# Kernel tuning notes

Measured on AMD Instinct MI355X. Metric: run time of the kernel, lower is better.

The kernel has to match this reference:

```python
import jax, jax.numpy as jnp
import numpy as np

L, D, H, DFF = 12, 768, 12, 3072
DH = D // H
EPS = 1e-5


def _layer_norm(x, g, b):
    # manual LN as in source: biased variance, eps inside sqrt
    mean = jnp.mean(x, axis=-1, keepdims=True)
    var = jnp.mean((x - mean) ** 2, axis=-1, keepdims=True)
    return g * (x - mean) / jnp.sqrt(var + EPS) + b


def setup_inputs() -> dict:
    key = jax.random.key(0)
    ks = jax.random.split(key, 10)
    x = jax.random.normal(ks[0], (8, 512, D), dtype=jnp.float32)
    mask = jnp.zeros((8, 1, 1, 512), dtype=jnp.float32)
    s = 0.02
    Wq = jax.random.normal(ks[1], (L, D, D), jnp.float32) * s
    Wk = jax.random.normal(ks[2], (L, D, D), jnp.float32) * s
    Wv = jax.random.normal(ks[3], (L, D, D), jnp.float32) * s
    Wo = jax.random.normal(ks[4], (L, D, D), jnp.float32) * s
    W1 = jax.random.normal(ks[5], (L, DFF, D), jnp.float32) * s
    W2 = jax.random.normal(ks[6], (L, D, DFF), jnp.float32) * s
    z = lambda *sh: jnp.zeros(sh, jnp.float32)
    o = lambda *sh: jnp.ones(sh, jnp.float32)
    return {
        'x': x, 'mask': mask,
        'Wq': Wq, 'bq': z(L, D), 'Wk': Wk, 'bk': z(L, D), 'Wv': Wv, 'bv': z(L, D),
        'Wo': Wo, 'bo': z(L, D), 'g1': o(L, D), 'b1': z(L, D),
        'W1': W1, 'bf1': z(L, DFF), 'W2': W2, 'bf2': z(L, D),
        'g2': o(L, D), 'b2': z(L, D),
    }


def reference(x, mask, Wq, bq, Wk, bk, Wv, bv, Wo, bo, g1, b1, W1, bf1, W2, bf2, g2, b2):
    B, S, _ = x.shape
    scale = 1.0 / jnp.sqrt(jnp.float32(DH))

    def layer(h, p):
        wq, pq, wk, pk, wv, pv, wo, po, gg1, bb1, w1, pf1, w2, pf2, gg2, bb2 = p
        # Dense: x @ W^T + b
        q = (h @ wq.T + pq).reshape(B, S, H, DH).transpose(0, 2, 1, 3)  # [B,H,S,dh]
        k = (h @ wk.T + pk).reshape(B, S, H, DH).transpose(0, 2, 1, 3)
        v = (h @ wv.T + pv).reshape(B, S, H, DH).transpose(0, 2, 1, 3)
        scores = jnp.einsum('bhqd,bhkd->bhqk', q, k) * scale
        scores = scores + mask * -1e9
        attn = jax.nn.softmax(scores, axis=-1)
        ctx = jnp.einsum('bhqk,bhkd->bhqd', attn, v)
        ctx = ctx.transpose(0, 2, 1, 3).reshape(B, S, D)
        a = _layer_norm(h + (ctx @ wo.T + po), gg1, bb1)
        ffn = jnp.maximum(a @ w1.T + pf1, 0.0) @ w2.T + pf2
        out = _layer_norm(a + ffn, gg2, bb2)
        return out, None

    params = (Wq, bq, Wk, bk, Wv, bv, Wo, bo, g1, b1, W1, bf1, W2, bf2, g2, b2)
    out, _ = jax.lax.scan(layer, x, params)
    return out
```

## Files before the change

kernel.cpp:

```cpp
#include <hip/hip_runtime.h>
#include <hip/hip_bf16.h>
#include <stdint.h>

#define DDIM 768
#define NH 12
#define DHD 64
#define DFF 3072
#define NLAYER 12
#define SEQ 512
#define NB 8
#define ROWS (NB*SEQ)
#define QS   2304

typedef __attribute__((ext_vector_type(4))) float f32x4;
typedef __attribute__((ext_vector_type(8))) short short8;

#define S_BARRIER()  asm volatile("s_barrier" ::: "memory")
#define WAIT_LGKM0() asm volatile("s_waitcnt lgkmcnt(0)" ::: "memory")
#define WAIT_VM0()   asm volatile("s_waitcnt vmcnt(0)" ::: "memory")
#define WAIT_VM3()   asm volatile("s_waitcnt vmcnt(3)" ::: "memory")
#define WAIT_VM4()   asm volatile("s_waitcnt vmcnt(4)" ::: "memory")
#define WAIT_VM6()   asm volatile("s_waitcnt vmcnt(6)" ::: "memory")

static __device__ __forceinline__ short bf16r(float f) {
  union { float f; uint32_t u; } a; a.f = f;
  uint32_t u = a.u;
  u += 0x7FFFu + ((u >> 16) & 1u);
  return (short)(u >> 16);
}

static __device__ __forceinline__ float bf2f(short s) {
  union { uint32_t u; float f; } c;
  c.u = ((uint32_t)(uint16_t)s) << 16;
  return c.f;
}

static __device__ __forceinline__ f32x4 mfma_bf16(short8 a, short8 b, f32x4 c) {
  return __builtin_amdgcn_mfma_f32_16x16x32_bf16(a, b, c, 0, 0, 0);
}

static __device__ __forceinline__ void gload16(const void* g, void* l) {
  __builtin_amdgcn_global_load_lds(
      (__attribute__((address_space(1))) void*)(void*)(uintptr_t)g,
      (__attribute__((address_space(3))) void*)l,
      16, 0, 0);
}

#define WDD    589824
#define WFD    2359296
#define WLAYER (4*WDD + 2*WFD)

struct WAll {
  const float* src[6];
  short* wb;
};

__global__ void wconv_all_kernel(WAll wa) {
  const int y = blockIdx.y;
  const int n8 = (y < 4) ? (WDD / 8) : (WFD / 8);
  const size_t perL   = (y < 4) ? WDD : WFD;
  const int    dstOff = (y < 4) ? y * WDD : 4 * WDD + (y - 4) * WFD;
  const float* __restrict__ src0 = wa.src[y];
  short* __restrict__ dst0 = wa.wb + dstOff;
  const int stride = gridDim.x * 256;
  const int start  = blockIdx.x * 256 + threadIdx.x;
  for (int l = 0; l < NLAYER; ++l) {
    const float* __restrict__ s = src0 + (size_t)l * perL;
    short* __restrict__ d = dst0 + (size_t)l * WLAYER;
    for (int i = start; i < n8; i += stride) {
      f32x4 a = *(const f32x4*)(s + (size_t)i * 8);
      f32x4 b = *(const f32x4*)(s + (size_t)i * 8 + 4);
      short8 o;
      o[0] = bf16r(a[0]); o[1] = bf16r(a[1]); o[2] = bf16r(a[2]); o[3] = bf16r(a[3]);
      o[4] = bf16r(b[0]); o[5] = bf16r(b[1]); o[6] = bf16r(b[2]); o[7] = bf16r(b[3]);
      *(short8*)(d + (size_t)i * 8) = o;
    }
  }
}

__global__ void xconv_kernel(const float* __restrict__ src, short* __restrict__ dst) {
  const int i = blockIdx.x * 256 + threadIdx.x;
  f32x4 a = *(const f32x4*)(src + (size_t)i * 8);
  f32x4 b = *(const f32x4*)(src + (size_t)i * 8 + 4);
  short8 o;
  o[0] = bf16r(a[0]); o[1] = bf16r(a[1]); o[2] = bf16r(a[2]); o[3] = bf16r(a[3]);
  o[4] = bf16r(b[0]); o[5] = bf16r(b[1]); o[6] = bf16r(b[2]); o[7] = bf16r(b[3]);
  *(short8*)(dst + (size_t)i * 8) = o;
}

__global__ void bcat_kernel(const float* __restrict__ bq, const float* __restrict__ bk,
                            const float* __restrict__ bv, float* __restrict__ out) {
  const int idx = blockIdx.x * 256 + threadIdx.x;
  if (idx >= NLAYER * QS) return;
  const int l = idx / QS;
  const int j = idx - l * QS;
  float v;
  if (j < DDIM)            v = bq[l * DDIM + j];
  else if (j < 2 * DDIM)   v = bk[l * DDIM + j - DDIM];
  else                     v = bv[l * DDIM + j - 2 * DDIM];
  out[idx] = v;
}

template<int OUTMODE, int BM>
__launch_bounds__(256, (BM == 256) ? 2 : 3)
__global__ void gemm_bt(const short* __restrict__ A, const short* __restrict__ W,
                        const float* __restrict__ bias, void* __restrict__ outp,
                        int M, int N, int K) {
  constexpr int MF  = BM / 32;
  constexpr int ISS = BM / 64;

  __shared__ __align__(16) short As[2][BM * 32];
  __shared__ __align__(16) short Bs[2][128 * 32];

  const int tid  = threadIdx.x;
  const int lane = tid & 63;
  const int wid  = tid >> 6;
  const int l16  = lane & 15;
  const int kg   = lane >> 4;
  const int wr   = wid >> 1;
  const int wc   = wid & 1;
  const int m0   = blockIdx.x * BM;
  const int n0   = blockIdx.y * 128;

  const f32x4 zero = {0.f, 0.f, 0.f, 0.f};
  f32x4 acc[MF][4];
  #pragma unroll
  for (int i = 0; i < MF; i++)
    #pragma unroll
    for (int j = 0; j < 4; j++) acc[i][j] = zero;

  const int lrow = lane >> 2;
  const int lcol = (lane & 3) * 8;
  const short* Ag = A + (size_t)(m0 + wid * (BM / 4) + lrow) * K + lcol;
  const short* Wg = W + (size_t)(n0 + wid * 32 + lrow) * K + lcol;

  auto stage = [&](int buf, int k0) {
    #pragma unroll
    for (int j = 0; j < ISS; j++)
      gload16(Ag + k0 + (size_t)(j * 16) * K, &As[buf][(wid * (BM / 4) + j * 16) * 32]);
    #pragma unroll
    for (int j = 0; j < 2; j++)
      gload16(Wg + k0 + (size_t)(j * 16) * K, &Bs[buf][(wid * 32 + j * 16) * 32]);
  };

  auto wait_tile = [&]() {
    if constexpr (ISS == 4) { WAIT_VM6(); }
    else if constexpr (ISS == 2) { WAIT_VM4(); }
    else { WAIT_VM3(); }
  };

  const int nsteps = K >> 5;
  stage(0, 0);
  stage(1, 32);
  wait_tile();
  S_BARRIER();

  for (int t = 0; t < nsteps; ++t) {
    const int cur = t & 1;
    short8 af[MF], bfr[4];
    #pragma unroll
    for (int i = 0; i < MF; i++)
      af[i] = *(const short8*)&As[cur][(wr * (BM / 2) + i * 16 + l16) * 32 + kg * 8];
    #pragma unroll
    for (int j = 0; j < 4; j++)
      bfr[j] = *(const short8*)&Bs[cur][(wc * 64 + j * 16 + l16) * 32 + kg * 8];
    WAIT_LGKM0();
    S_BARRIER();

    const bool pf = (t + 2 < nsteps);
    if (pf) stage(cur, (t + 2) << 5);
    __builtin_amdgcn_sched_barrier(0);
    #pragma unroll
    for (int i = 0; i < MF; i++)
      #pragma unroll
      for (int j = 0; j < 4; j++)
        acc[i][j] = mfma_bf16(af[i], bfr[j], acc[i][j]);
    __builtin_amdgcn_sched_barrier(0);

    if (pf) { wait_tile(); }
    else    { WAIT_VM0(); }
    S_BARRIER();
  }

  float* outf = (float*)outp;
  short* outb = (short*)outp;
  #pragma unroll
  for (int j = 0; j < 4; j++) {
    const int col = n0 + wc * 64 + j * 16 + l16;
    const float bv = bias[col];
    #pragma unroll
    for (int i = 0; i < MF; i++) {
      const int row0 = m0 + wr * (BM / 2) + i * 16 + kg * 4;
      #pragma unroll
      for (int e = 0; e < 4; e++) {
        float v = acc[i][j][e] + bv;
        if (OUTMODE == 2) v = fmaxf(v, 0.0f);
        const size_t off = (size_t)(row0 + e) * N + col;
        if (OUTMODE == 0) outf[off] = v;
        else              outb[off] = bf16r(v);
      }
    }
  }
}

__launch_bounds__(256, 2)
__global__ void attn_kernel(const short* __restrict__ QKV, const float* __restrict__ mask,
                            short* __restrict__ ctx) {
  __shared__ __align__(16) short Vt[64 * 512];

  const int bh = blockIdx.x;
  const int b = bh / NH;
  const int h = bh % NH;
  const int tid  = threadIdx.x;
  const int lane = tid & 63;
  const int wid  = tid >> 6;
  const int l16  = lane & 15;
  const int kg   = lane >> 4;

  const short* Qb = QKV + (size_t)b * SEQ * QS + h * DHD;
  const short* Kb = Qb + DDIM;
  const short* Vb = Qb + 2 * DDIM;

  for (int c = tid; c < SEQ * 8; c += 256) {
    const int kv = c >> 3;
    const int d0 = (c & 7) * 8;
    short8 v = *(const short8*)(Vb + (size_t)kv * QS + d0);
    #pragma unroll
    for (int j = 0; j < 8; j++)
      Vt[(d0 + j) * 512 + (kv ^ ((j & 3) << 3))] = v[j];
  }
  __syncthreads();

  const int q0 = blockIdx.y * 128 + wid * 32;

  short8 qf[2][2];
  #pragma unroll
  for (int rt = 0; rt < 2; rt++)
    #pragma unroll
    for (int dh = 0; dh < 2; dh++)
      qf[rt][dh] = *(const short8*)(Qb + (size_t)(q0 + rt * 16 + l16) * QS + dh * 32 + kg * 8);

  float mrun[2] = {-1e30f, -1e30f};
  float lrun[2] = {0.0f, 0.0f};
  const f32x4 zero = {0.f, 0.f, 0.f, 0.f};
  f32x4 oacc[2][4];
  #pragma unroll
  for (int rt = 0; rt < 2; rt++)
    #pragma unroll
    for (int dt = 0; dt < 4; dt++) oacc[rt][dt] = zero;

  const float* maskb = mask + (size_t)b * SEQ;

  for (int kv0 = 0; kv0 < SEQ; kv0 += 32) {
    short8 kf[2][2];
    #pragma unroll
    for (int kvh = 0; kvh < 2; kvh++)
      #pragma unroll
      for (int dh = 0; dh < 2; dh++)
        kf[kvh][dh] = *(const short8*)(Kb + (size_t)(kv0 + kvh * 16 + l16) * QS + dh * 32 + kg * 8);

    short8 vf[4];
    #pragma unroll
    for (int dt = 0; dt < 4; dt++) {
      const int d = dt * 16 + l16;
      vf[dt] = *(const short8*)&Vt[d * 512 + ((kv0 + kg * 8) ^ ((d & 3) << 3))];
    }

    const f32x4 mq0 = *(const f32x4*)(maskb + kv0 + kg * 4);
    const f32x4 mq1 = *(const f32x4*)(maskb + kv0 + 16 + kg * 4);

    #pragma unroll
    for (int rt = 0; rt < 2; rt++) {
      f32x4 s0 = zero, s1 = zero;
      __builtin_amdgcn_s_setprio(1);
      s0 = mfma_bf16(kf[0][0], qf[rt][0], s0);
      s0 = mfma_bf16(kf[0][1], qf[rt][1], s0);
      s1 = mfma_bf16(kf[1][0], qf[rt][0], s1);
      s1 = mfma_bf16(kf[1][1], qf[rt][1], s1);
      __builtin_amdgcn_s_setprio(0);

      float p[8];
      #pragma unroll
      for (int e = 0; e < 4; e++) {
        p[e]     = s0[e] * 0.125f + mq0[e] * (-1e9f);
        p[e + 4] = s1[e] * 0.125f + mq1[e] * (-1e9f);
      }
      float mt = p[0];
      #pragma unroll
      for (int e = 1; e < 8; e++) mt = fmaxf(mt, p[e]);
      mt = fmaxf(mt, __shfl_xor(mt, 16, 64));
      mt = fmaxf(mt, __shfl_xor(mt, 32, 64));
      const float mnew = fmaxf(mrun[rt], mt);
      const float corr = __expf(mrun[rt] - mnew);
      float ts = 0.0f;
      #pragma unroll
      for (int e = 0; e < 8; e++) { p[e] = __expf(p[e] - mnew); ts += p[e]; }
      ts += __shfl_xor(ts, 16, 64);
      ts += __shfl_xor(ts, 32, 64);
      lrun[rt] = lrun[rt] * corr + ts;
      mrun[rt] = mnew;

      const int P0 = (int)(((uint32_t)(uint16_t)bf16r(p[1]) << 16) | (uint16_t)bf16r(p[0]));
      const int P1 = (int)(((uint32_t)(uint16_t)bf16r(p[3]) << 16) | (uint16_t)bf16r(p[2]));
      const int P2 = (int)(((uint32_t)(uint16_t)bf16r(p[5]) << 16) | (uint16_t)bf16r(p[4]));
      const int P3 = (int)(((uint32_t)(uint16_t)bf16r(p[7]) << 16) | (uint16_t)bf16r(p[6]));
      const int sl0 = (((2 * kg) & 3) << 4) + l16;
      const int sl1 = (((2 * kg + 1) & 3) << 4) + l16;
      const int x0 = __shfl(P0, sl0, 64), y0 = __shfl(P2, sl0, 64);
      const int x1 = __shfl(P1, sl0, 64), y1 = __shfl(P3, sl0, 64);
      const int x2 = __shfl(P0, sl1, 64), y2 = __shfl(P2, sl1, 64);
      const int x3 = __shfl(P1, sl1, 64), y3 = __shfl(P3, sl1, 64);
      union { int w[4]; short8 v; } pa;
      const bool hi = (kg >= 2);
      pa.w[0] = hi ? y0 : x0;
      pa.w[1] = hi ? y1 : x1;
      pa.w[2] = hi ? y2 : x2;
      pa.w[3] = hi ? y3 : x3;

      const float c0 = __shfl(corr, kg * 4 + 0, 64);
      const float c1 = __shfl(corr, kg * 4 + 1, 64);
      const float c2 = __shfl(corr, kg * 4 + 2, 64);
      const float c3 = __shfl(corr, kg * 4 + 3, 64);

      __builtin_amdgcn_s_setprio(1);
      #pragma unroll
      for (int dt = 0; dt < 4; dt++) {
        f32x4 o = oacc[rt][dt];
        o[0] *= c0; o[1] *= c1; o[2] *= c2; o[3] *= c3;
        oacc[rt][dt] = mfma_bf16(pa.v, vf[dt], o);
      }
      __builtin_amdgcn_s_setprio(0);
    }
  }

  short* cb = ctx + (size_t)b * SEQ * DDIM + h * DHD;
  #pragma unroll
  for (int rt = 0; rt < 2; rt++) {
    const float li = 1.0f / lrun[rt];
    const float l0 = __shfl(li, kg * 4 + 0, 64);
    const float l1 = __shfl(li, kg * 4 + 1, 64);
    const float l2 = __shfl(li, kg * 4 + 2, 64);
    const float l3 = __shfl(li, kg * 4 + 3, 64);
    #pragma unroll
    for (int dt = 0; dt < 4; dt++) {
      const f32x4 o = oacc[rt][dt];
      const int col = dt * 16 + l16;
      const size_t base = (size_t)(q0 + rt * 16 + kg * 4) * DDIM + col;
      cb[base + 0 * DDIM] = bf16r(o[0] * l0);
      cb[base + 1 * DDIM] = bf16r(o[1] * l1);
      cb[base + 2 * DDIM] = bf16r(o[2] * l2);
      cb[base + 3 * DDIM] = bf16r(o[3] * l3);
    }
  }
}

__launch_bounds__(256, 4)
__global__ void ln_kernel(const float* __restrict__ resid, const short* __restrict__ projv,
                          const float* __restrict__ gw, const float* __restrict__ bw,
                          float* __restrict__ outf, short* __restrict__ outb) {
  const int lane = threadIdx.x & 63;
  const int wid  = threadIdx.x >> 6;
  const int row  = blockIdx.x * 4 + wid;
  const float* rp = resid + (size_t)row * DDIM;
  float v[12];
  float s = 0.0f;
  #pragma unroll
  for (int c = 0; c < 12; c++) {
    const float pv = bf2f(projv[(size_t)row * DDIM + c * 64 + lane]);
    v[c] = rp[c * 64 + lane] + pv;
    s += v[c];
  }
  #pragma unroll
  for (int o = 1; o < 64; o <<= 1) s += __shfl_xor(s, o, 64);
  const float mean = s * (1.0f / 768.0f);
  float q = 0.0f;
  #pragma unroll
  for (int c = 0; c < 12; c++) { const float d = v[c] - mean; q += d * d; }
  #pragma unroll
  for (int o = 1; o < 64; o <<= 1) q += __shfl_xor(q, o, 64);
  const float inv = 1.0f / sqrtf(q * (1.0f / 768.0f) + 1e-5f);
  #pragma unroll
  for (int c = 0; c < 12; c++) {
    const int idx = c * 64 + lane;
    const float y = gw[idx] * (v[c] - mean) * inv + bw[idx];
    outf[(size_t)row * DDIM + idx] = y;
    outb[(size_t)row * DDIM + idx] = bf16r(y);
  }
}

extern "C" void kernel_launch(void* const* d_in, const int* in_sizes, int n_in,
                              void* d_out, int out_size, void* d_ws, size_t ws_size,
                              hipStream_t stream) {
  const float* x    = (const float*)d_in[0];
  const float* mask = (const float*)d_in[1];
  const float* Wq   = (const float*)d_in[2];
  const float* bq   = (const float*)d_in[3];
  const float* Wk   = (const float*)d_in[4];
  const float* bk   = (const float*)d_in[5];
  const float* Wv   = (const float*)d_in[6];
  const float* bv   = (const float*)d_in[7];
  const float* Wo   = (const float*)d_in[8];
  const float* bo   = (const float*)d_in[9];
  const float* g1   = (const float*)d_in[10];
  const float* b1   = (const float*)d_in[11];
  const float* W1   = (const float*)d_in[12];
  const float* bf1  = (const float*)d_in[13];
  const float* W2   = (const float*)d_in[14];
  const float* bf2  = (const float*)d_in[15];
  const float* g2   = (const float*)d_in[16];
  const float* b2   = (const float*)d_in[17];

  const size_t SD = (size_t)ROWS * DDIM;

  char* ws = (char*)d_ws;
  float* H0   = (float*)ws;  ws += SD * 4;
  short* Bbuf = (short*)ws;  ws += SD * 2;
  short* QKVb = (short*)ws;  ws += (size_t)ROWS * QS * 2;
  short* Cb   = (short*)ws;  ws += SD * 2;
  short* Pb   = (short*)ws;  ws += SD * 2;
  short* F1   = (short*)ws;  ws += (size_t)ROWS * DFF * 2;
  float* Bqkv = (float*)ws;  ws += (size_t)NLAYER * QS * 4;
  short* WB   = (short*)ws;

  {
    WAll wa{};
    wa.src[0] = Wq; wa.src[1] = Wk; wa.src[2] = Wv; wa.src[3] = Wo;
    wa.src[4] = W1; wa.src[5] = W2;
    wa.wb = WB;
    wconv_all_kernel<<<dim3(1152, 6), 256, 0, stream>>>(wa);
    xconv_kernel<<<dim3((int)(SD / 8 / 256)), 256, 0, stream>>>(x, Bbuf);
    bcat_kernel<<<dim3((NLAYER * QS + 255) / 256), 256, 0, stream>>>(bq, bk, bv, Bqkv);
  }

  for (int l = 0; l < NLAYER; l++) {
    const short* WL = WB + (size_t)l * WLAYER;

    gemm_bt<1, 256><<<dim3(16, 18), 256, 0, stream>>>(
        Bbuf, WL, Bqkv + (size_t)l * QS, QKVb, ROWS, QS, DDIM);

    attn_kernel<<<dim3(NB * NH, 4), 256, 0, stream>>>(QKVb, mask, Cb);

    gemm_bt<1, 64><<<dim3(64, 6), 256, 0, stream>>>(
        Cb, WL + 3 * WDD, bo + (size_t)l * DDIM, Pb, ROWS, DDIM, DDIM);

    ln_kernel<<<dim3(ROWS / 4), 256, 0, stream>>>(l ? H0 : x, Pb,
                                                  g1 + (size_t)l * DDIM, b1 + (size_t)l * DDIM,
                                                  H0, Bbuf);

    gemm_bt<2, 256><<<dim3(16, 24), 256, 0, stream>>>(
        Bbuf, WL + 4 * WDD, bf1 + (size_t)l * DFF, F1, ROWS, DFF, DDIM);

    gemm_bt<1, 64><<<dim3(64, 6), 256, 0, stream>>>(
        F1, WL + 4 * WDD + WFD, bf2 + (size_t)l * DDIM, Pb, ROWS, DDIM, DFF);

    ln_kernel<<<dim3(ROWS / 4), 256, 0, stream>>>(H0, Pb,
                                                  g2 + (size_t)l * DDIM, b2 + (size_t)l * DDIM,
                                                  (l == NLAYER - 1) ? (float*)d_out : H0,
                                                  Bbuf);
  }
}
```

Before: 2.273 ms.

## Split QKV into separate buffers, keep residual in bf16, vectorize layernorm

Replaces the fused QKV output buffer with separate Q, K, V buffers written by one z-batched GEMM launch, so the bias-concatenation kernel goes away and attention reads rows with a DDIM stride. The residual stream is now stored only in bf16 instead of fp32, and layernorm uses packed two-element loads and stores, writing fp32 only on the last layer. GEMM tiles for QKV and FFN1 drop from BM=256 to BM=128 with a higher occupancy target. Keeping the residual in bf16 cuts memory traffic but adds rounding error that accumulates across layers.

```diff
diff --git a/kernel.cpp b/kernel.cpp
--- a/kernel.cpp
+++ b/kernel.cpp
@@ -10,9 +10,9 @@
 #define SEQ 512
 #define NB 8
 #define ROWS (NB*SEQ)
-#define QS   2304
 
 typedef __attribute__((ext_vector_type(4))) float f32x4;
+typedef __attribute__((ext_vector_type(2))) float f32x2;
 typedef __attribute__((ext_vector_type(8))) short short8;
 
 #define S_BARRIER()  asm volatile("s_barrier" ::: "memory")
@@ -20,7 +20,6 @@
 #define WAIT_VM0()   asm volatile("s_waitcnt vmcnt(0)" ::: "memory")
 #define WAIT_VM3()   asm volatile("s_waitcnt vmcnt(3)" ::: "memory")
 #define WAIT_VM4()   asm volatile("s_waitcnt vmcnt(4)" ::: "memory")
-#define WAIT_VM6()   asm volatile("s_waitcnt vmcnt(6)" ::: "memory")
 
 static __device__ __forceinline__ short bf16r(float f) {
   union { float f; uint32_t u; } a; a.f = f;
@@ -88,26 +87,22 @@
   *(short8*)(dst + (size_t)i * 8) = o;
 }
 
-__global__ void bcat_kernel(const float* __restrict__ bq, const float* __restrict__ bk,
-                            const float* __restrict__ bv, float* __restrict__ out) {
-  const int idx = blockIdx.x * 256 + threadIdx.x;
-  if (idx >= NLAYER * QS) return;
-  const int l = idx / QS;
-  const int j = idx - l * QS;
-  float v;
-  if (j < DDIM)            v = bq[l * DDIM + j];
-  else if (j < 2 * DDIM)   v = bk[l * DDIM + j - DDIM];
-  else                     v = bv[l * DDIM + j - 2 * DDIM];
-  out[idx] = v;
-}
+struct GemmB {
+  const short* W0; const short* W1; const short* W2;
+  const float* b0; const float* b1; const float* b2;
+  short* o0; short* o1; short* o2;
+};
 
 template<int OUTMODE, int BM>
-__launch_bounds__(256, (BM == 256) ? 2 : 3)
-__global__ void gemm_bt(const short* __restrict__ A, const short* __restrict__ W,
-                        const float* __restrict__ bias, void* __restrict__ outp,
-                        int M, int N, int K) {
+__launch_bounds__(256, 3)
+__global__ void gemm_bt(const short* __restrict__ A, GemmB gb, int M, int N, int K) {
   constexpr int MF  = BM / 32;
   constexpr int ISS = BM / 64;
+
+  const int z = blockIdx.z;
+  const short* W    = (z == 0) ? gb.W0 : ((z == 1) ? gb.W1 : gb.W2);
+  const float* bias = (z == 0) ? gb.b0 : ((z == 1) ? gb.b1 : gb.b2);
+  short* outb       = (z == 0) ? gb.o0 : ((z == 1) ? gb.o1 : gb.o2);
 
   __shared__ __align__(16) short As[2][BM * 32];
   __shared__ __align__(16) short Bs[2][128 * 32];
@@ -143,16 +138,10 @@
       gload16(Wg + k0 + (size_t)(j * 16) * K, &Bs[buf][(wid * 32 + j * 16) * 32]);
   };
 
-  auto wait_tile = [&]() {
-    if constexpr (ISS == 4) { WAIT_VM6(); }
-    else if constexpr (ISS == 2) { WAIT_VM4(); }
-    else { WAIT_VM3(); }
-  };
-
   const int nsteps = K >> 5;
   stage(0, 0);
   stage(1, 32);
-  wait_tile();
+  if (ISS == 2) { WAIT_VM4(); } else { WAIT_VM3(); }
   S_BARRIER();
 
   for (int t = 0; t < nsteps; ++t) {
@@ -177,13 +166,11 @@
         acc[i][j] = mfma_bf16(af[i], bfr[j], acc[i][j]);
     __builtin_amdgcn_sched_barrier(0);
 
-    if (pf) { wait_tile(); }
+    if (pf) { if (ISS == 2) { WAIT_VM4(); } else { WAIT_VM3(); } }
     else    { WAIT_VM0(); }
     S_BARRIER();
   }
 
-  float* outf = (float*)outp;
-  short* outb = (short*)outp;
   #pragma unroll
   for (int j = 0; j < 4; j++) {
     const int col = n0 + wc * 64 + j * 16 + l16;
@@ -195,16 +182,15 @@
       for (int e = 0; e < 4; e++) {
         float v = acc[i][j][e] + bv;
         if (OUTMODE == 2) v = fmaxf(v, 0.0f);
-        const size_t off = (size_t)(row0 + e) * N + col;
-        if (OUTMODE == 0) outf[off] = v;
-        else              outb[off] = bf16r(v);
+        outb[(size_t)(row0 + e) * N + col] = bf16r(v);
       }
     }
   }
 }
 
 __launch_bounds__(256, 2)
-__global__ void attn_kernel(const short* __restrict__ QKV, const float* __restrict__ mask,
+__global__ void attn_kernel(const short* __restrict__ Qg, const short* __restrict__ Kg,
+                            const short* __restrict__ Vg, const float* __restrict__ mask,
                             short* __restrict__ ctx) {
   __shared__ __align__(16) short Vt[64 * 512];
 
@@ -217,14 +203,14 @@
   const int l16  = lane & 15;
   const int kg   = lane >> 4;
 
-  const short* Qb = QKV + (size_t)b * SEQ * QS + h * DHD;
-  const short* Kb = Qb + DDIM;
-  const short* Vb = Qb + 2 * DDIM;
+  const short* Qb = Qg + (size_t)b * SEQ * DDIM + h * DHD;
+  const short* Kb = Kg + (size_t)b * SEQ * DDIM + h * DHD;
+  const short* Vb = Vg + (size_t)b * SEQ * DDIM + h * DHD;
 
   for (int c = tid; c < SEQ * 8; c += 256) {
     const int kv = c >> 3;
     const int d0 = (c & 7) * 8;
-    short8 v = *(const short8*)(Vb + (size_t)kv * QS + d0);
+    short8 v = *(const short8*)(Vb + (size_t)kv * DDIM + d0);
     #pragma unroll
     for (int j = 0; j < 8; j++)
       Vt[(d0 + j) * 512 + (kv ^ ((j & 3) << 3))] = v[j];
@@ -238,7 +224,7 @@
   for (int rt = 0; rt < 2; rt++)
     #pragma unroll
     for (int dh = 0; dh < 2; dh++)
-      qf[rt][dh] = *(const short8*)(Qb + (size_t)(q0 + rt * 16 + l16) * QS + dh * 32 + kg * 8);
+      qf[rt][dh] = *(const short8*)(Qb + (size_t)(q0 + rt * 16 + l16) * DDIM + dh * 32 + kg * 8);
 
   float mrun[2] = {-1e30f, -1e30f};
   float lrun[2] = {0.0f, 0.0f};
@@ -257,7 +243,7 @@
     for (int kvh = 0; kvh < 2; kvh++)
       #pragma unroll
       for (int dh = 0; dh < 2; dh++)
-        kf[kvh][dh] = *(const short8*)(Kb + (size_t)(kv0 + kvh * 16 + l16) * QS + dh * 32 + kg * 8);
+        kf[kvh][dh] = *(const short8*)(Kb + (size_t)(kv0 + kvh * 16 + l16) * DDIM + dh * 32 + kg * 8);
 
     short8 vf[4];
     #pragma unroll
@@ -354,21 +340,27 @@
   }
 }
 
+template<int OUTF32>
 __launch_bounds__(256, 4)
-__global__ void ln_kernel(const float* __restrict__ resid, const short* __restrict__ projv,
+__global__ void ln_kernel(const short* __restrict__ resid, const short* __restrict__ proj,
                           const float* __restrict__ gw, const float* __restrict__ bw,
-                          float* __restrict__ outf, short* __restrict__ outb) {
+                          short* __restrict__ outb, float* __restrict__ outf) {
   const int lane = threadIdx.x & 63;
   const int wid  = threadIdx.x >> 6;
   const int row  = blockIdx.x * 4 + wid;
-  const float* rp = resid + (size_t)row * DDIM;
+  const short* rp = resid + (size_t)row * DDIM;
+  const short* pp = proj  + (size_t)row * DDIM;
   float v[12];
   float s = 0.0f;
   #pragma unroll
-  for (int c = 0; c < 12; c++) {
-    const float pv = bf2f(projv[(size_t)row * DDIM + c * 64 + lane]);
-    v[c] = rp[c * 64 + lane] + pv;
-    s += v[c];
+  for (int c = 0; c < 6; c++) {
+    const int col = c * 128 + lane * 2;
+    const uint32_t ur = *(const uint32_t*)(rp + col);
+    const uint32_t up = *(const uint32_t*)(pp + col);
+    const float a0 = bf2f((short)(ur & 0xffff)) + bf2f((short)(up & 0xffff));
+    const float a1 = bf2f((short)(ur >> 16))    + bf2f((short)(up >> 16));
+    v[2 * c] = a0; v[2 * c + 1] = a1;
+    s += a0 + a1;
   }
   #pragma unroll
   for (int o = 1; o < 64; o <<= 1) s += __shfl_xor(s, o, 64);
@@ -380,11 +372,18 @@
   for (int o = 1; o < 64; o <<= 1) q += __shfl_xor(q, o, 64);
   const float inv = 1.0f / sqrtf(q * (1.0f / 768.0f) + 1e-5f);
   #pragma unroll
-  for (int c = 0; c < 12; c++) {
-    const int idx = c * 64 + lane;
-    const float y = gw[idx] * (v[c] - mean) * inv + bw[idx];
-    outf[(size_t)row * DDIM + idx] = y;
-    outb[(size_t)row * DDIM + idx] = bf16r(y);
+  for (int c = 0; c < 6; c++) {
+    const int col = c * 128 + lane * 2;
+    const f32x2 g2 = *(const f32x2*)(gw + col);
+    const f32x2 b2 = *(const f32x2*)(bw + col);
+    const float y0 = g2[0] * (v[2 * c] - mean) * inv + b2[0];
+    const float y1 = g2[1] * (v[2 * c + 1] - mean) * inv + b2[1];
+    const uint32_t pk = ((uint32_t)(uint16_t)bf16r(y1) << 16) | (uint16_t)bf16r(y0);
+    *(uint32_t*)(outb + (size_t)row * DDIM + col) = pk;
+    if (OUTF32) {
+      f32x2 o2 = {y0, y1};
+      *(f32x2*)(outf + (size_t)row * DDIM + col) = o2;
+    }
   }
 }
 
@@ -413,14 +412,15 @@
   const size_t SD = (size_t)ROWS * DDIM;
 
   char* ws = (char*)d_ws;
-  float* H0   = (float*)ws;  ws += SD * 4;
-  short* Bbuf = (short*)ws;  ws += SD * 2;
-  short* QKVb = (short*)ws;  ws += (size_t)ROWS * QS * 2;
-  short* Cb   = (short*)ws;  ws += SD * 2;
-  short* Pb   = (short*)ws;  ws += SD * 2;
-  short* F1   = (short*)ws;  ws += (size_t)ROWS * DFF * 2;
-  float* Bqkv = (float*)ws;  ws += (size_t)NLAYER * QS * 4;
-  short* WB   = (short*)ws;
+  short* hb = (short*)ws;  ws += SD * 2;
+  short* ab = (short*)ws;  ws += SD * 2;
+  short* Qb = (short*)ws;  ws += SD * 2;
+  short* Kb = (short*)ws;  ws += SD * 2;
+  short* Vb = (short*)ws;  ws += SD * 2;
+  short* Cb = (short*)ws;  ws += SD * 2;
+  short* Pb = (short*)ws;  ws += SD * 2;
+  short* F1 = (short*)ws;  ws += (size_t)ROWS * DFF * 2;
+  short* WB = (short*)ws;
 
   {
     WAll wa{};
@@ -428,34 +428,51 @@
     wa.src[4] = W1; wa.src[5] = W2;
     wa.wb = WB;
     wconv_all_kernel<<<dim3(1152, 6), 256, 0, stream>>>(wa);
-    xconv_kernel<<<dim3((int)(SD / 8 / 256)), 256, 0, stream>>>(x, Bbuf);
-    bcat_kernel<<<dim3((NLAYER * QS + 255) / 256), 256, 0, stream>>>(bq, bk, bv, Bqkv);
+    xconv_kernel<<<dim3((int)(SD / 8 / 256)), 256, 0, stream>>>(x, hb);
   }
 
   for (int l = 0; l < NLAYER; l++) {
     const short* WL = WB + (size_t)l * WLAYER;
 
-    gemm_bt<1, 256><<<dim3(16, 18), 256, 0, stream>>>(
-        Bbuf, WL, Bqkv + (size_t)l * QS, QKVb, ROWS, QS, DDIM);
-
-    attn_kernel<<<dim3(NB * NH, 4), 256, 0, stream>>>(QKVb, mask, Cb);
-
-    gemm_bt<1, 64><<<dim3(64, 6), 256, 0, stream>>>(
-        Cb, WL + 3 * WDD, bo + (size_t)l * DDIM, Pb, ROWS, DDIM, DDIM);
-
-    ln_kernel<<<dim3(ROWS / 4), 256, 0, stream>>>(l ? H0 : x, Pb,
-                                                  g1 + (size_t)l * DDIM, b1 + (size_t)l * DDIM,
-                                                  H0, Bbuf);
-
-    gemm_bt<2, 256><<<dim3(16, 24), 256, 0, stream>>>(
-        Bbuf, WL + 4 * WDD, bf1 + (size_t)l * DFF, F1, ROWS, DFF, DDIM);
-
-    gemm_bt<1, 64><<<dim3(64, 6), 256, 0, stream>>>(
-        F1, WL + 4 * WDD + WFD, bf2 + (size_t)l * DDIM, Pb, ROWS, DDIM, DFF);
-
-    ln_kernel<<<dim3(ROWS / 4), 256, 0, stream>>>(H0, Pb,
-                                                  g2 + (size_t)l * DDIM, b2 + (size_t)l * DDIM,
-                                                  (l == NLAYER - 1) ? (float*)d_out : H0,
-                                                  Bbuf);
-  }
-}
+    {
+      GemmB g{};
+      g.W0 = WL;           g.b0 = bq + (size_t)l * DDIM; g.o0 = Qb;
+      g.W1 = WL + WDD;     g.b1 = bk + (size_t)l * DDIM; g.o1 = Kb;
+      g.W2 = WL + 2 * WDD; g.b2 = bv + (size_t)l * DDIM; g.o2 = Vb;
+      gemm_bt<1, 128><<<dim3(32, 6, 3), 256, 0, stream>>>(hb, g, ROWS, DDIM, DDIM);
+    }
+
+    attn_kernel<<<dim3(NB * NH, 4), 256, 0, stream>>>(Qb, Kb, Vb, mask, Cb);
+
+    {
+      GemmB g{};
+      g.W0 = WL + 3 * WDD; g.b0 = bo + (size_t)l * DDIM; g.o0 = Pb;
+      gemm_bt<1, 64><<<dim3(64, 6, 1), 256, 0, stream>>>(Cb, g, ROWS, DDIM, DDIM);
+    }
+
+    ln_kernel<0><<<dim3(ROWS / 4), 256, 0, stream>>>(hb, Pb,
+                                                     g1 + (size_t)l * DDIM, b1 + (size_t)l * DDIM,
+                                                     ab, nullptr);
+
+    {
+      GemmB g{};
+      g.W0 = WL + 4 * WDD; g.b0 = bf1 + (size_t)l * DFF; g.o0 = F1;
+      gemm_bt<2, 128><<<dim3(32, 24, 1), 256, 0, stream>>>(ab, g, ROWS, DFF, DDIM);
+    }
+
+    {
+      GemmB g{};
+      g.W0 = WL + 4 * WDD + WFD; g.b0 = bf2 + (size_t)l * DDIM; g.o0 = Pb;
+      gemm_bt<1, 64><<<dim3(64, 6, 1), 256, 0, stream>>>(F1, g, ROWS, DDIM, DFF);
+    }
+
+    if (l == NLAYER - 1)
+      ln_kernel<1><<<dim3(ROWS / 4), 256, 0, stream>>>(ab, Pb,
+                                                       g2 + (size_t)l * DDIM, b2 + (size_t)l * DDIM,
+                                                       hb, (float*)d_out);
+    else
+      ln_kernel<0><<<dim3(ROWS / 4), 256, 0, stream>>>(ab, Pb,
+                                                       g2 + (size_t)l * DDIM, b2 + (size_t)l * DDIM,
+                                                       hb, nullptr);
+  }
+}
```

Result: faster. 2.149 ms (-5.5%).
